# Performance work log

Measured on AMD Instinct MI355X. Metric: run time of the kernel, lower is better.

The kernel has to match this reference:

```python
import jax, jax.numpy as jnp
import numpy as np

B, S, DM = 2, 2048, 1024
H, HD = 16, 64  # heads, head_dims = dims // heads
SCALE = HD ** -0.5


def softmax_one(x):
    # softmax with +1 in the denominator: exp(x_i) / (1 + sum_j exp(x_j))
    # stable form: shift by m = max(max(x), 0)
    m = jnp.maximum(jnp.max(x, axis=-1, keepdims=True), 0.0)
    e = jnp.exp(x - m)
    return e / (jnp.exp(-m) + jnp.sum(e, axis=-1, keepdims=True))


def setup_inputs() -> dict:
    key = jax.random.key(0)
    ks = jax.random.split(key, 11)
    init = lambda k, shape, fan_in: jax.random.uniform(k, shape, jnp.float32, -1.0, 1.0) * (fan_in ** -0.5)
    return {
        "query": jax.random.normal(ks[0], (B, S, DM), jnp.float32),
        "key": jax.random.normal(ks[1], (B, S, DM), jnp.float32),
        "value": jax.random.normal(ks[2], (B, S, DM), jnp.float32),
        "Wq": init(ks[3], (H * HD, DM), DM), "bq": init(ks[4], (H * HD,), DM),
        "Wk": init(ks[5], (H * HD, DM), DM), "bk": init(ks[6], (H * HD,), DM),
        "Wv": init(ks[7], (H * HD, DM), DM), "bv": init(ks[8], (H * HD,), DM),
        "Wo": init(ks[9], (DM, H * HD), H * HD), "bo": init(ks[10], (DM,), H * HD),
    }


def _proj(x, W, b):
    # [B,S,DM] -> [B,H,S,HD]
    y = x @ W.T + b
    return y.reshape(B, S, H, HD).transpose(0, 2, 1, 3)


def reference(query, key, value, Wq, bq, Wk, bk, Wv, bv, Wo, bo):
    Q = _proj(query, Wq, bq)
    K = _proj(key, Wk, bk)
    V = _proj(value, Wv, bv)
    scores = jnp.einsum("bhqd,bhkd->bhqk", Q, K) * SCALE  # [B,H,S,S]
    attn = softmax_one(scores)
    out = jnp.einsum("bhqk,bhkd->bhqd", attn, V)  # [B,H,S,HD]
    out = out.transpose(0, 2, 1, 3).reshape(B, S, H * HD)
    return out @ Wo.T + bo
```

## Files before the change

kernel.cpp:

```cpp
#include <hip/hip_runtime.h>

#define B_ 2
#define S_ 2048
#define DM_ 1024
#define H_ 16
#define HD_ 64
#define QSCALE_ 0.18033688011112042f

typedef __bf16 bf16;
typedef __attribute__((ext_vector_type(4))) __bf16 bf16x4;
typedef __attribute__((ext_vector_type(8))) __bf16 bf16x8;
typedef __attribute__((ext_vector_type(4))) float f32x4;

#define MFMA16(a, b, c) __builtin_amdgcn_mfma_f32_16x16x32_bf16((a), (b), (c), 0, 0, 0)
#define EXP2(x) __builtin_amdgcn_exp2f(x)

__device__ __forceinline__ void async16(const bf16* g, bf16* l) {
  __builtin_amdgcn_global_load_lds(
      (const __attribute__((address_space(1))) void*)g,
      (__attribute__((address_space(3))) void*)l, 16, 0, 0);
}

__global__ __launch_bounds__(256) void convert_kernel(
    const float* __restrict__ q, const float* __restrict__ k,
    const float* __restrict__ v, const float* __restrict__ wq,
    const float* __restrict__ wk, const float* __restrict__ wv,
    const float* __restrict__ wo, bf16* __restrict__ dst) {
  size_t idx = ((size_t)blockIdx.x * 256 + threadIdx.x) * 8;
  const float* src;
  size_t off;
  if (idx < 4194304) { src = q; off = idx; }
  else if (idx < 8388608) { src = k; off = idx - 4194304; }
  else if (idx < 12582912) { src = v; off = idx - 8388608; }
  else if (idx < 13631488) { src = wq; off = idx - 12582912; }
  else if (idx < 14680064) { src = wk; off = idx - 13631488; }
  else if (idx < 15728640) { src = wv; off = idx - 14680064; }
  else { src = wo; off = idx - 15728640; }
  float4 a = *(const float4*)(src + off);
  float4 b = *(const float4*)(src + off + 4);
  bf16x8 o;
  o[0] = (bf16)a.x; o[1] = (bf16)a.y; o[2] = (bf16)a.z; o[3] = (bf16)a.w;
  o[4] = (bf16)b.x; o[5] = (bf16)b.y; o[6] = (bf16)b.z; o[7] = (bf16)b.w;
  *(bf16x8*)(dst + idx) = o;
}

template <int MODE>
__device__ __forceinline__ void gemm_body(bf16* smem, const bf16* A,
                                          const bf16* W, const float* bias,
                                          bf16* C, float scale, int m0,
                                          int n0) {
  constexpr int K = 1024;
  bf16* As = smem;
  bf16* Bs = smem + 128 * 64;
  const int t = threadIdx.x;
  const int lane = t & 63, wave = t >> 6;
  const int quad = lane >> 4, l16 = lane & 15;
  const int wm = (wave >> 1) * 64, wn = (wave & 1) * 64;

  const f32x4 zero = {0.f, 0.f, 0.f, 0.f};
  f32x4 acc[4][4];
  for (int i = 0; i < 4; i++)
    for (int j = 0; j < 4; j++) acc[i][j] = zero;

  for (int k0 = 0; k0 < K; k0 += 64) {
    for (int i = 0; i < 4; ++i) {
      int c = i * 256 + t;
      int row = c >> 3, g = c & 7;
      int off = k0 + ((g ^ (row & 7)) * 8);
      async16(A + (size_t)(m0 + row) * K + off, As + c * 8);
      async16(W + (size_t)(n0 + row) * K + off, Bs + c * 8);
    }
    __syncthreads();

    for (int ks = 0; ks < 2; ks++) {
      bf16x8 af[4], bfr[4];
      for (int mb = 0; mb < 4; mb++) {
        int ra = wm + mb * 16 + l16;
        af[mb] = *(const bf16x8*)(As + ra * 64 + ((ks * 4 + quad) ^ (ra & 7)) * 8);
        int rb = wn + mb * 16 + l16;
        bfr[mb] = *(const bf16x8*)(Bs + rb * 64 + ((ks * 4 + quad) ^ (rb & 7)) * 8);
      }
      for (int mb = 0; mb < 4; mb++)
        for (int nb = 0; nb < 4; nb++)
          acc[mb][nb] = MFMA16(af[mb], bfr[nb], acc[mb][nb]);
    }
    __syncthreads();
  }

  if constexpr (MODE == 2) {
    bf16* Ct = smem;
    for (int nb = 0; nb < 4; nb++) {
      int cl = wn + nb * 16 + l16;
      float bv = bias[n0 + cl] * scale;
      for (int mb = 0; mb < 4; mb++) {
        int rowb = wm + mb * 16 + quad * 4;
        bf16x4 v;
        for (int r = 0; r < 4; r++)
          v[r] = (bf16)(acc[mb][nb][r] * scale + bv);
        *(bf16x4*)(Ct + cl * 136 + rowb) = v;
      }
    }
    __syncthreads();
    int c = t >> 1, half = t & 1;
    int colg = n0 + c;
    int hh = colg >> 6, dd = colg & 63;
    int bb = m0 >> 11, s0 = m0 & (S_ - 1);
    bf16* dst = C + (((size_t)(bb * H_ + hh)) * HD_ + dd) * S_ + s0 + half * 64;
    const bf16* srcr = Ct + c * 136 + half * 64;
    for (int j = 0; j < 8; ++j)
      *(bf16x8*)(dst + j * 8) = *(const bf16x8*)(srcr + j * 8);
  } else {
    for (int nb = 0; nb < 4; nb++) {
      int col = n0 + wn + nb * 16 + l16;
      float bv = bias[col] * scale;
      for (int mb = 0; mb < 4; mb++) {
        int rowb = m0 + wm + mb * 16 + quad * 4;
        for (int r = 0; r < 4; r++) {
          int row = rowb + r;
          float o = acc[mb][nb][r] * scale + bv;
          int bb = row >> 11, s = row & (S_ - 1);
          int h = col >> 6, d = col & 63;
          C[(((size_t)(bb * H_ + h)) * S_ + s) * HD_ + d] = (bf16)o;
        }
      }
    }
  }
}

__global__ __launch_bounds__(256, 4) void qkv_proj_kernel(
    const bf16* Xc, const float* bq, const float* bk, const float* bv,
    bf16* Qo, bf16* Ko, bf16* Vo) {
  __shared__ __align__(16) bf16 smem[128 * 136];
  int bid = blockIdx.x;
  int z = bid >> 8;
  int r = bid & 255;
  int c = r & 7;
  int j = r >> 3;
  int m0 = (c * 4 + (j & 3)) * 128;
  int n0 = (j >> 2) * 128;
  const bf16* A = Xc + (size_t)z * 4194304;
  const bf16* W = Xc + 12582912 + (size_t)z * 1048576;
  if (z == 0)
    gemm_body<1>(smem, A, W, bq, Qo, QSCALE_, m0, n0);
  else if (z == 1)
    gemm_body<1>(smem, A, W, bk, Ko, 1.0f, m0, n0);
  else
    gemm_body<2>(smem, A, W, bv, Vo, 1.0f, m0, n0);
}

__global__ __launch_bounds__(256, 4) void out_proj_kernel(const bf16* A,
                                                          const bf16* W,
                                                          const float* bias,
                                                          float* C) {
  constexpr int K = 1024, N = 1024;
  __shared__ __align__(16) bf16 As[64 * 64];
  __shared__ __align__(16) bf16 Bs[64 * 64];
  const int t = threadIdx.x;
  const int lane = t & 63, wave = t >> 6;
  const int quad = lane >> 4, l16 = lane & 15;
  int bid = blockIdx.x;
  int c = bid & 7;
  int j = bid >> 3;
  const int m0 = (c * 8 + (j & 7)) * 64;
  const int n0 = (j >> 3) * 64;

  const f32x4 zero = {0.f, 0.f, 0.f, 0.f};
  f32x4 acc[4];
  for (int i = 0; i < 4; i++) acc[i] = zero;

  for (int k0 = 0; k0 < K; k0 += 64) {
    for (int i = 0; i < 2; ++i) {
      int cc = i * 256 + t;
      int row = cc >> 3, g = cc & 7;
      int off = k0 + ((g ^ (row & 7)) * 8);
      async16(A + (size_t)(m0 + row) * K + off, As + cc * 8);
      async16(W + (size_t)(n0 + row) * K + off, Bs + cc * 8);
    }
    __syncthreads();

    for (int ks = 0; ks < 2; ks++) {
      int ra = wave * 16 + l16;
      bf16x8 af = *(const bf16x8*)(As + ra * 64 + ((ks * 4 + quad) ^ (ra & 7)) * 8);
      for (int nb = 0; nb < 4; nb++) {
        int rb = nb * 16 + l16;
        bf16x8 bfr =
            *(const bf16x8*)(Bs + rb * 64 + ((ks * 4 + quad) ^ (rb & 7)) * 8);
        acc[nb] = MFMA16(af, bfr, acc[nb]);
      }
    }
    __syncthreads();
  }

  for (int nb = 0; nb < 4; nb++) {
    int col = n0 + nb * 16 + l16;
    float bv = bias[col];
    int rowb = m0 + wave * 16 + quad * 4;
    for (int r = 0; r < 4; r++)
      C[(size_t)(rowb + r) * N + col] = acc[nb][r] + bv;
  }
}

__global__ __launch_bounds__(512, 4) void attn_kernel(
    const bf16* __restrict__ Q, const bf16* __restrict__ Kg,
    const bf16* __restrict__ VTg, bf16* __restrict__ O) {
  __shared__ __align__(16) bf16 smem[26624];
  const int t = threadIdx.x;
  const int lane = t & 63, wave = t >> 6;
  const int quad = lane >> 4, l16 = lane & 15;
  const int qh = wave >> 2;
  const int kq = wave & 3;
  const int id = blockIdx.x;
  const int bh = id & 31;
  const int qt = id >> 5;
  const int q0 = qt * 64;
  const int b = bh >> 4, h = bh & 15;
  const size_t base = ((size_t)(b * H_ + h)) * S_ * HD_;
  const bf16* Qp = Q + base;
  const bf16* Kp = Kg + base;
  const bf16* Vp = VTg + base;

  bf16* Ks = smem;
  bf16* Vt = smem + 8192;
  bf16* Pw = smem + 16384 + wave * (32 * 40);

  bf16x8 aq[2][2];
  for (int s = 0; s < 2; s++) {
    const bf16* qr = Qp + (size_t)(q0 + qh * 32 + s * 16 + l16) * HD_;
    aq[s][0] = *(const bf16x8*)(qr + quad * 8);
    aq[s][1] = *(const bf16x8*)(qr + 32 + quad * 8);
  }

  const f32x4 zero = {0.f, 0.f, 0.f, 0.f};
  f32x4 oc[2][4];
  for (int s = 0; s < 2; s++)
    for (int d = 0; d < 4; d++) oc[s][d] = zero;
  float rs[2] = {0.f, 0.f};

  for (int kv0 = 0; kv0 < S_; kv0 += 128) {
    for (int i = 0; i < 2; ++i) {
      int cc = i * 512 + t;
      int row = cc >> 3, g = cc & 7;
      async16(Kp + (size_t)(kv0 + row) * HD_ + (g ^ (row & 7)) * 8,
              Ks + cc * 8);
    }
    for (int i = 0; i < 2; ++i) {
      int cc = i * 512 + t;
      int d = cc >> 4, g = cc & 15;
      async16(Vp + (size_t)d * S_ + kv0 + (g ^ (d & 15)) * 8, Vt + cc * 8);
    }
    __syncthreads();

    f32x4 sc[2][2];
    for (int s = 0; s < 2; s++)
      for (int nb = 0; nb < 2; nb++) sc[s][nb] = zero;
    for (int ks = 0; ks < 2; ks++) {
      for (int nb = 0; nb < 2; nb++) {
        int row = kq * 32 + nb * 16 + l16;
        int slot = (ks * 4 + quad) ^ (row & 7);
        bf16x8 kf = *(const bf16x8*)(Ks + row * 64 + slot * 8);
        for (int s = 0; s < 2; s++)
          sc[s][nb] = MFMA16(kf, aq[s][ks], sc[s][nb]);
      }
    }

    for (int s = 0; s < 2; s++) {
      bf16* prow = Pw + (s * 16 + l16) * 40 + quad * 4;
      for (int nb = 0; nb < 2; nb++) {
        float p0 = EXP2(sc[s][nb][0]);
        float p1 = EXP2(sc[s][nb][1]);
        float p2 = EXP2(sc[s][nb][2]);
        float p3 = EXP2(sc[s][nb][3]);
        rs[s] += (p0 + p1) + (p2 + p3);
        bf16x4 pv = {(bf16)p0, (bf16)p1, (bf16)p2, (bf16)p3};
        *(bf16x4*)(prow + nb * 16) = pv;
      }
    }

    bf16x8 vf[4];
    for (int db = 0; db < 4; db++) {
      int row = db * 16 + l16;
      int g = kq * 4 + quad;
      vf[db] = *(const bf16x8*)(Vt + row * 128 + (g ^ (row & 15)) * 8);
    }
    for (int s = 0; s < 2; s++) {
      bf16x8 ap = *(const bf16x8*)(Pw + (s * 16 + l16) * 40 + quad * 8);
      for (int db = 0; db < 4; db++)
        oc[s][db] = MFMA16(ap, vf[db], oc[s][db]);
    }

    __syncthreads();
  }

  float rtot[2];
  for (int s = 0; s < 2; s++) {
    float v = rs[s];
    v += __shfl_xor(v, 16);
    v += __shfl_xor(v, 32);
    rtot[s] = v;
  }

  float* Ld = (float*)smem;
  float* rsL = (float*)(smem + 17408);

  if (kq & 1) {
    float* Lw = Ld + (size_t)((qh * 2 + (kq >> 1)) * 32) * 68;
    for (int s = 0; s < 2; s++) {
      for (int db = 0; db < 4; db++)
        for (int r = 0; r < 4; r++)
          Lw[(s * 16 + quad * 4 + r) * 68 + db * 16 + l16] = oc[s][db][r];
      if (quad == 0) rsL[(qh * 2 + (kq >> 1)) * 32 + s * 16 + l16] = rtot[s];
    }
  }
  __syncthreads();
  if (!(kq & 1)) {
    float* Lr = Ld + (size_t)((qh * 2 + (kq >> 1)) * 32) * 68;
    for (int s = 0; s < 2; s++) {
      for (int db = 0; db < 4; db++)
        for (int r = 0; r < 4; r++)
          oc[s][db][r] += Lr[(s * 16 + quad * 4 + r) * 68 + db * 16 + l16];
      rtot[s] += rsL[(qh * 2 + (kq >> 1)) * 32 + s * 16 + l16];
    }
  }
  if (kq == 2) {
    float* Lw = Ld + (size_t)((qh * 2 + 1) * 32) * 68;
    for (int s = 0; s < 2; s++) {
      for (int db = 0; db < 4; db++)
        for (int r = 0; r < 4; r++)
          Lw[(s * 16 + quad * 4 + r) * 68 + db * 16 + l16] = oc[s][db][r];
      if (quad == 0) rsL[(qh * 2 + 1) * 32 + s * 16 + l16] = rtot[s];
    }
  }
  __syncthreads();
  if (kq == 0) {
    float* Lr = Ld + (size_t)((qh * 2 + 1) * 32) * 68;
    for (int s = 0; s < 2; s++) {
      float l_all = 1.f + rtot[s] + rsL[(qh * 2 + 1) * 32 + s * 16 + l16];
      for (int r = 0; r < 4; r++) {
        float inv = 1.f / __shfl(l_all, quad * 4 + r);
        int qrow = q0 + qh * 32 + s * 16 + quad * 4 + r;
        size_t orow = ((size_t)(b * S_ + qrow) * H_ + h) * HD_;
        for (int db = 0; db < 4; db++) {
          float val = oc[s][db][r] +
                      Lr[(s * 16 + quad * 4 + r) * 68 + db * 16 + l16];
          O[orow + db * 16 + l16] = (bf16)(val * inv);
        }
      }
    }
  }
}

extern "C" void kernel_launch(void* const* d_in, const int* in_sizes, int n_in,
                              void* d_out, int out_size, void* d_ws,
                              size_t ws_size, hipStream_t stream) {
  const float* query = (const float*)d_in[0];
  const float* key = (const float*)d_in[1];
  const float* value = (const float*)d_in[2];
  const float* bq = (const float*)d_in[4];
  const float* bk = (const float*)d_in[6];
  const float* bv = (const float*)d_in[8];
  const float* bo = (const float*)d_in[10];
  float* out = (float*)d_out;

  bf16* Xc = (bf16*)d_ws;
  bf16* Qw = Xc + 16777216;
  const size_t SZ = (size_t)B_ * H_ * S_ * HD_;
  bf16* Kw = Qw + SZ;
  bf16* Vw = Kw + SZ;
  bf16* Ow = Vw + SZ;

  convert_kernel<<<8192, 256, 0, stream>>>(query, key, value,
                                           (const float*)d_in[3],
                                           (const float*)d_in[5],
                                           (const float*)d_in[7],
                                           (const float*)d_in[9], Xc);
  qkv_proj_kernel<<<768, 256, 0, stream>>>(Xc, bq, bk, bv, Qw, Kw, Vw);
  attn_kernel<<<1024, 512, 0, stream>>>(Qw, Kw, Vw, Ow);
  out_proj_kernel<<<1024, 256, 0, stream>>>(Ow, Xc + 15728640, bo, out);
}
```

Measured before the change: 221.8 us.

## Load K/V fragments directly from global memory and halve attention block size

The attention kernel drops the shared-memory staging of K and V tiles and their per-iteration barriers. Each wave now reads K and V fragments straight from global memory into registers, relying on caches for reuse. Blocks shrink from 8 to 4 waves, each wave covering 64 keys per step instead of 32, so the cross-wave reduction of partial outputs is simpler. The trade-off is more global/L2 traffic, uncoalesced strided V reads, and no data reuse through LDS, in exchange for less synchronisation and LDS usage.

```diff
diff --git a/kernel.cpp b/kernel.cpp
--- a/kernel.cpp
+++ b/kernel.cpp
@@ -200,15 +200,15 @@
   }
 }
 
-__global__ __launch_bounds__(512, 4) void attn_kernel(
+__global__ __launch_bounds__(256, 4) void attn_kernel(
     const bf16* __restrict__ Q, const bf16* __restrict__ Kg,
     const bf16* __restrict__ VTg, bf16* __restrict__ O) {
-  __shared__ __align__(16) bf16 smem[26624];
+  __shared__ __align__(16) bf16 smem[9216];
   const int t = threadIdx.x;
   const int lane = t & 63, wave = t >> 6;
   const int quad = lane >> 4, l16 = lane & 15;
-  const int qh = wave >> 2;
-  const int kq = wave & 3;
+  const int qh = wave >> 1;
+  const int kh = wave & 1;
   const int id = blockIdx.x;
   const int bh = id & 31;
   const int qt = id >> 5;
@@ -219,10 +219,6 @@
   const bf16* Kp = Kg + base;
   const bf16* Vp = VTg + base;
 
-  bf16* Ks = smem;
-  bf16* Vt = smem + 8192;
-  bf16* Pw = smem + 16384 + wave * (32 * 40);
-
   bf16x8 aq[2][2];
   for (int s = 0; s < 2; s++) {
     const bf16* qr = Qp + (size_t)(q0 + qh * 32 + s * 16 + l16) * HD_;
@@ -236,36 +232,27 @@
     for (int d = 0; d < 4; d++) oc[s][d] = zero;
   float rs[2] = {0.f, 0.f};
 
+  bf16* Pw = smem + wave * (32 * 72);
+
   for (int kv0 = 0; kv0 < S_; kv0 += 128) {
-    for (int i = 0; i < 2; ++i) {
-      int cc = i * 512 + t;
-      int row = cc >> 3, g = cc & 7;
-      async16(Kp + (size_t)(kv0 + row) * HD_ + (g ^ (row & 7)) * 8,
-              Ks + cc * 8);
-    }
-    for (int i = 0; i < 2; ++i) {
-      int cc = i * 512 + t;
-      int d = cc >> 4, g = cc & 15;
-      async16(Vp + (size_t)d * S_ + kv0 + (g ^ (d & 15)) * 8, Vt + cc * 8);
-    }
-    __syncthreads();
-
-    f32x4 sc[2][2];
+    const bf16* Kt = Kp + (size_t)(kv0 + kh * 64) * HD_;
+    const bf16* Vt = Vp + kv0 + kh * 64;
+
+    f32x4 sc[2][4];
     for (int s = 0; s < 2; s++)
-      for (int nb = 0; nb < 2; nb++) sc[s][nb] = zero;
+      for (int nb = 0; nb < 4; nb++) sc[s][nb] = zero;
     for (int ks = 0; ks < 2; ks++) {
-      for (int nb = 0; nb < 2; nb++) {
-        int row = kq * 32 + nb * 16 + l16;
-        int slot = (ks * 4 + quad) ^ (row & 7);
-        bf16x8 kf = *(const bf16x8*)(Ks + row * 64 + slot * 8);
+      for (int nb = 0; nb < 4; nb++) {
+        bf16x8 kf = *(const bf16x8*)(Kt + (size_t)(nb * 16 + l16) * HD_ +
+                                     ks * 32 + quad * 8);
         for (int s = 0; s < 2; s++)
           sc[s][nb] = MFMA16(kf, aq[s][ks], sc[s][nb]);
       }
     }
 
     for (int s = 0; s < 2; s++) {
-      bf16* prow = Pw + (s * 16 + l16) * 40 + quad * 4;
-      for (int nb = 0; nb < 2; nb++) {
+      bf16* prow = Pw + (s * 16 + l16) * 72 + quad * 4;
+      for (int nb = 0; nb < 4; nb++) {
         float p0 = EXP2(sc[s][nb][0]);
         float p1 = EXP2(sc[s][nb][1]);
         float p2 = EXP2(sc[s][nb][2]);
@@ -276,19 +263,18 @@
       }
     }
 
-    bf16x8 vf[4];
-    for (int db = 0; db < 4; db++) {
-      int row = db * 16 + l16;
-      int g = kq * 4 + quad;
-      vf[db] = *(const bf16x8*)(Vt + row * 128 + (g ^ (row & 15)) * 8);
-    }
-    for (int s = 0; s < 2; s++) {
-      bf16x8 ap = *(const bf16x8*)(Pw + (s * 16 + l16) * 40 + quad * 8);
+    for (int ks2 = 0; ks2 < 2; ks2++) {
+      bf16x8 vf[4];
       for (int db = 0; db < 4; db++)
-        oc[s][db] = MFMA16(ap, vf[db], oc[s][db]);
-    }
-
-    __syncthreads();
+        vf[db] = *(const bf16x8*)(Vt + (size_t)(db * 16 + l16) * S_ +
+                                  ks2 * 32 + quad * 8);
+      for (int s = 0; s < 2; s++) {
+        bf16x8 ap = *(const bf16x8*)(Pw + (s * 16 + l16) * 72 + ks2 * 32 +
+                                     quad * 8);
+        for (int db = 0; db < 4; db++)
+          oc[s][db] = MFMA16(ap, vf[db], oc[s][db]);
+      }
+    }
   }
 
   float rtot[2];
@@ -299,42 +285,23 @@
     rtot[s] = v;
   }
 
+  __syncthreads();
   float* Ld = (float*)smem;
-  float* rsL = (float*)(smem + 17408);
-
-  if (kq & 1) {
-    float* Lw = Ld + (size_t)((qh * 2 + (kq >> 1)) * 32) * 68;
+  float* rsL = (float*)(smem + 8704);
+  if (kh) {
+    float* Lw = Ld + (size_t)(qh * 32) * 68;
     for (int s = 0; s < 2; s++) {
+      if (quad == 0) rsL[qh * 32 + s * 16 + l16] = rtot[s];
       for (int db = 0; db < 4; db++)
         for (int r = 0; r < 4; r++)
           Lw[(s * 16 + quad * 4 + r) * 68 + db * 16 + l16] = oc[s][db][r];
-      if (quad == 0) rsL[(qh * 2 + (kq >> 1)) * 32 + s * 16 + l16] = rtot[s];
     }
   }
   __syncthreads();
-  if (!(kq & 1)) {
-    float* Lr = Ld + (size_t)((qh * 2 + (kq >> 1)) * 32) * 68;
+  if (!kh) {
+    float* Lr = Ld + (size_t)(qh * 32) * 68;
     for (int s = 0; s < 2; s++) {
-      for (int db = 0; db < 4; db++)
-        for (int r = 0; r < 4; r++)
-          oc[s][db][r] += Lr[(s * 16 + quad * 4 + r) * 68 + db * 16 + l16];
-      rtot[s] += rsL[(qh * 2 + (kq >> 1)) * 32 + s * 16 + l16];
-    }
-  }
-  if (kq == 2) {
-    float* Lw = Ld + (size_t)((qh * 2 + 1) * 32) * 68;
-    for (int s = 0; s < 2; s++) {
-      for (int db = 0; db < 4; db++)
-        for (int r = 0; r < 4; r++)
-          Lw[(s * 16 + quad * 4 + r) * 68 + db * 16 + l16] = oc[s][db][r];
-      if (quad == 0) rsL[(qh * 2 + 1) * 32 + s * 16 + l16] = rtot[s];
-    }
-  }
-  __syncthreads();
-  if (kq == 0) {
-    float* Lr = Ld + (size_t)((qh * 2 + 1) * 32) * 68;
-    for (int s = 0; s < 2; s++) {
-      float l_all = 1.f + rtot[s] + rsL[(qh * 2 + 1) * 32 + s * 16 + l16];
+      float l_all = 1.f + rtot[s] + rsL[qh * 32 + s * 16 + l16];
       for (int r = 0; r < 4; r++) {
         float inv = 1.f / __shfl(l_all, quad * 4 + r);
         int qrow = q0 + qh * 32 + s * 16 + quad * 4 + r;
@@ -374,6 +341,6 @@
                                            (const float*)d_in[7],
                                            (const float*)d_in[9], Xc);
   qkv_proj_kernel<<<768, 256, 0, stream>>>(Xc, bq, bk, bv, Qw, Kw, Vw);
-  attn_kernel<<<1024, 512, 0, stream>>>(Qw, Kw, Vw, Ow);
+  attn_kernel<<<1024, 256, 0, stream>>>(Qw, Kw, Vw, Ow);
   out_proj_kernel<<<1024, 256, 0, stream>>>(Ow, Xc + 15728640, bo, out);
 }
```

Result: slower. 287.7 us (+29.7%).
